# Performance work log

Measured on AMD Instinct MI355X. Metric: run time of the kernel, lower is better.

The kernel has to match this reference:

```python
import jax, jax.numpy as jnp
import numpy as np

N_PIXELS = 262144
N_CENTERS = 1024
N_G = 256

def setup_inputs() -> dict:
    key = jax.random.key(0)
    k1, k2, k3, k4, k5 = jax.random.split(key, 5)
    return {
        "alphas": jax.random.normal(k1, (N_CENTERS, 1), dtype=jnp.float32),
        "betas": jax.random.normal(k2, (N_G, 2), dtype=jnp.float32) * 0.1,
        "K": jax.random.normal(k3, (N_PIXELS, N_G), dtype=jnp.float32) * 0.05,
        "all_pixels": jax.random.normal(k4, (N_PIXELS, 2), dtype=jnp.float32),
        "all_p_centers": jax.random.normal(k5, (N_CENTERS, 2), dtype=jnp.float32),
        "sdp2": jnp.ones((), dtype=jnp.float32) * 2.0,
    }

def reference(alphas, betas, K, all_pixels, all_p_centers, sdp2):
    # deformed pixel coordinates: (n_pixels, 2)
    deformed = all_pixels - K @ betas
    # pairwise squared distances via norm expansion (same math as the torch
    # ones-matmul broadcasting, expressed with plain broadcasting):
    p_norm2 = jnp.sum(jnp.square(deformed), axis=1, keepdims=True)      # (n_pixels, 1)
    c_norm2 = jnp.sum(jnp.square(all_p_centers), axis=1)                # (n_centers,)
    p_dot_c = 2.0 * (deformed @ all_p_centers.T)                        # (n_pixels, n_centers)
    big_matrix = p_norm2 + c_norm2[None, :] - p_dot_c
    kBp = jnp.exp(-big_matrix / (2.0 * sdp2))
    return kBp @ alphas                                                  # (n_pixels, 1)
```

## Files before the change

### kernel.cpp

```cpp
#include <hip/hip_runtime.h>

#if defined(__has_builtin)
#  if __has_builtin(__builtin_amdgcn_exp2f)
#    define EXP2F(x) __builtin_amdgcn_exp2f(x)
#  else
#    define EXP2F(x) exp2f(x)
#  endif
#else
#  define EXP2F(x) exp2f(x)
#endif

constexpr int NPIX  = 262144;
constexpr int NC    = 1024;
constexpr int NG    = 256;
constexpr int BLOCK = 256;
constexpr int PIX_PER_BLOCK = BLOCK * 2;

template <int CTRL>
__device__ __forceinline__ float dpp_add(float v) {
    union { float f; int i; } u, t;
    u.f = v;
    t.i = __builtin_amdgcn_update_dpp(0, u.i, CTRL, 0xF, 0xF, true);
    return v + t.f;
}
__device__ __forceinline__ float sum16(float v) {
    v = dpp_add<0xB1>(v);
    v = dpp_add<0x4E>(v);
    v = dpp_add<0x141>(v);
    v = dpp_add<0x140>(v);
    return v;
}

__global__ __launch_bounds__(BLOCK, 2)
void kbpa_fused(const float* __restrict__ alphas,
                const float* __restrict__ betas,
                const float* __restrict__ K,
                const float* __restrict__ pixels,
                const float* __restrict__ centers,
                const float* __restrict__ sdp2p,
                float* __restrict__ out)
{
    __shared__ float4 cpack[NC];

    const int tid  = threadIdx.x;
    const int lane = tid & 63;
    const int wave = tid >> 6;
    const int l4   = lane & 15;
    const int lg   = lane >> 4;
    const int own  = l4 * 4 + lg;

    const float f   = -1.44269504088896340736f / (2.0f * sdp2p[0]);
    const float m2f = -2.0f * f;

    for (int c = tid; c < NC; c += BLOCK) {
        const float cx = centers[2 * c + 0];
        const float cy = centers[2 * c + 1];
        cpack[c] = make_float4(cx, cy, alphas[c] * EXP2F(f * (cx * cx + cy * cy)), 0.f);
    }

    const float4* bf4 = (const float4*)betas;
    float4 b0[4], b1[4];
    #pragma unroll
    for (int k = 0; k < 4; ++k) {
        b0[k] = bf4[l4 * 2 + k * 32];
        b1[k] = bf4[l4 * 2 + k * 32 + 1];
    }

    const int blockBase = blockIdx.x * PIX_PER_BLOCK;
    const int g0 = blockBase + wave * 64;
    const int g1 = g0 + BLOCK;

    const float2* pix2 = (const float2*)pixels;
    const float2 pixA = pix2[g0 + own];
    const float2 pixB = pix2[g1 + own];

    float dxA = 0.f, dyA = 0.f, dxB = 0.f, dyB = 0.f;
    #pragma unroll 2
    for (int it = 0; it < 16; ++it) {
        const float4* kr = (const float4*)(K + (size_t)(g0 + it * 4 + lg) * NG);
        float4 kv[4];
        #pragma unroll
        for (int k = 0; k < 4; ++k) kv[k] = kr[l4 + 16 * k];
        float sx = 0.f, sy = 0.f;
        #pragma unroll
        for (int k = 0; k < 4; ++k) {
            sx = fmaf(kv[k].x, b0[k].x, sx); sy = fmaf(kv[k].x, b0[k].y, sy);
            sx = fmaf(kv[k].y, b0[k].z, sx); sy = fmaf(kv[k].y, b0[k].w, sy);
            sx = fmaf(kv[k].z, b1[k].x, sx); sy = fmaf(kv[k].z, b1[k].y, sy);
            sx = fmaf(kv[k].w, b1[k].z, sx); sy = fmaf(kv[k].w, b1[k].w, sy);
        }
        sx = sum16(sx); sy = sum16(sy);
        if (l4 == it) { dxA = pixA.x - sx; dyA = pixA.y - sy; }
    }
    #pragma unroll 2
    for (int it = 0; it < 16; ++it) {
        const float4* kr = (const float4*)(K + (size_t)(g1 + it * 4 + lg) * NG);
        float4 kv[4];
        #pragma unroll
        for (int k = 0; k < 4; ++k) kv[k] = kr[l4 + 16 * k];
        float sx = 0.f, sy = 0.f;
        #pragma unroll
        for (int k = 0; k < 4; ++k) {
            sx = fmaf(kv[k].x, b0[k].x, sx); sy = fmaf(kv[k].x, b0[k].y, sy);
            sx = fmaf(kv[k].y, b0[k].z, sx); sy = fmaf(kv[k].y, b0[k].w, sy);
            sx = fmaf(kv[k].z, b1[k].x, sx); sy = fmaf(kv[k].z, b1[k].y, sy);
            sx = fmaf(kv[k].w, b1[k].z, sx); sy = fmaf(kv[k].w, b1[k].w, sy);
        }
        sx = sum16(sx); sy = sum16(sy);
        if (l4 == it) { dxB = pixB.x - sx; dyB = pixB.y - sy; }
    }

    __syncthreads();

    const float dxs0 = m2f * dxA, dys0 = m2f * dyA;
    const float dxs1 = m2f * dxB, dys1 = m2f * dyB;
    const float pn0  = f * (dxA * dxA + dyA * dyA);
    const float pn1  = f * (dxB * dxB + dyB * dyB);
    float acc0 = 0.f, acc1 = 0.f;
    #pragma unroll 8
    for (int c = 0; c < NC; ++c) {
        const float4 cp = cpack[c];
        const float e0 = EXP2F(fmaf(dxs0, cp.x, dys0 * cp.y));
        const float e1 = EXP2F(fmaf(dxs1, cp.x, dys1 * cp.y));
        acc0 = fmaf(cp.z, e0, acc0);
        acc1 = fmaf(cp.z, e1, acc1);
    }
    out[g0 + own] = acc0 * EXP2F(pn0);
    out[g1 + own] = acc1 * EXP2F(pn1);
}

extern "C" void kernel_launch(void* const* d_in, const int* in_sizes, int n_in,
                              void* d_out, int out_size, void* d_ws, size_t ws_size,
                              hipStream_t stream)
{
    const float* alphas  = (const float*)d_in[0];
    const float* betas   = (const float*)d_in[1];
    const float* K       = (const float*)d_in[2];
    const float* pixels  = (const float*)d_in[3];
    const float* centers = (const float*)d_in[4];
    const float* sdp2    = (const float*)d_in[5];
    float* outp          = (float*)d_out;

    hipLaunchKernelGGL(kbpa_fused, dim3(NPIX / PIX_PER_BLOCK), dim3(BLOCK), 0, stream,
                       alphas, betas, K, pixels, centers, sdp2, outp);
}
```

Before: 85.02 us.

## Hold centers in registers and rotate pixels across lanes systolically

```diff
diff --git a/kernel.cpp b/kernel.cpp
--- a/kernel.cpp
+++ b/kernel.cpp
@@ -31,31 +31,70 @@
     return v;
 }
 
+__global__ void prep_centers(const float* __restrict__ alphas,
+                             const float* __restrict__ centers,
+                             const float* __restrict__ sdp2p,
+                             float* __restrict__ ws)
+{
+    const int c = blockIdx.x * blockDim.x + threadIdx.x;
+    if (c < NC) {
+        const float f  = -1.44269504088896340736f / (2.0f * sdp2p[0]);
+        const float cx = centers[2 * c + 0];
+        const float cy = centers[2 * c + 1];
+        ws[c]          = cx;
+        ws[NC + c]     = cy;
+        ws[2 * NC + c] = alphas[c] * EXP2F(f * (cx * cx + cy * cy));
+    }
+}
+
+__device__ __forceinline__ float systolic_b(float dx, float dy, float m2f,
+                                            const float4 rcx[4], const float4 rcy[4],
+                                            const float4 rca[4], int src)
+{
+    float dxs = m2f * dx, dys = m2f * dy, acc = 0.f;
+    for (int t = 0; t < 64; ++t) {
+        #pragma unroll
+        for (int jj = 0; jj < 4; ++jj) {
+            acc = fmaf(rca[jj].x, EXP2F(fmaf(dxs, rcx[jj].x, dys * rcy[jj].x)), acc);
+            acc = fmaf(rca[jj].y, EXP2F(fmaf(dxs, rcx[jj].y, dys * rcy[jj].y)), acc);
+            acc = fmaf(rca[jj].z, EXP2F(fmaf(dxs, rcx[jj].z, dys * rcy[jj].z)), acc);
+            acc = fmaf(rca[jj].w, EXP2F(fmaf(dxs, rcx[jj].w, dys * rcy[jj].w)), acc);
+        }
+        dxs = __shfl(dxs, src);
+        dys = __shfl(dys, src);
+        acc = __shfl(acc, src);
+    }
+    return acc;
+}
+
 __global__ __launch_bounds__(BLOCK, 2)
-void kbpa_fused(const float* __restrict__ alphas,
-                const float* __restrict__ betas,
-                const float* __restrict__ K,
-                const float* __restrict__ pixels,
-                const float* __restrict__ centers,
-                const float* __restrict__ sdp2p,
-                float* __restrict__ out)
+void kbpa_main(const float* __restrict__ betas,
+               const float* __restrict__ K,
+               const float* __restrict__ pixels,
+               const float* __restrict__ sdp2p,
+               const float* __restrict__ ws,
+               float* __restrict__ out)
 {
-    __shared__ float4 cpack[NC];
-
     const int tid  = threadIdx.x;
     const int lane = tid & 63;
     const int wave = tid >> 6;
     const int l4   = lane & 15;
     const int lg   = lane >> 4;
     const int own  = l4 * 4 + lg;
+    const int src  = (lane + 1) & 63;
 
     const float f   = -1.44269504088896340736f / (2.0f * sdp2p[0]);
     const float m2f = -2.0f * f;
 
-    for (int c = tid; c < NC; c += BLOCK) {
-        const float cx = centers[2 * c + 0];
-        const float cy = centers[2 * c + 1];
-        cpack[c] = make_float4(cx, cy, alphas[c] * EXP2F(f * (cx * cx + cy * cy)), 0.f);
+    const float4* wcx4 = (const float4*)(ws);
+    const float4* wcy4 = (const float4*)(ws + NC);
+    const float4* wca4 = (const float4*)(ws + 2 * NC);
+    float4 rcx[4], rcy[4], rca[4];
+    #pragma unroll
+    for (int jj = 0; jj < 4; ++jj) {
+        rcx[jj] = wcx4[lane * 4 + jj];
+        rcy[jj] = wcy4[lane * 4 + jj];
+        rca[jj] = wca4[lane * 4 + jj];
     }
 
     const float4* bf4 = (const float4*)betas;
@@ -74,7 +113,7 @@
     const float2 pixA = pix2[g0 + own];
     const float2 pixB = pix2[g1 + own];
 
-    float dxA = 0.f, dyA = 0.f, dxB = 0.f, dyB = 0.f;
+    float dx0 = 0.f, dy0 = 0.f, dx1 = 0.f, dy1 = 0.f;
     #pragma unroll 2
     for (int it = 0; it < 16; ++it) {
         const float4* kr = (const float4*)(K + (size_t)(g0 + it * 4 + lg) * NG);
@@ -90,8 +129,13 @@
             sx = fmaf(kv[k].w, b1[k].z, sx); sy = fmaf(kv[k].w, b1[k].w, sy);
         }
         sx = sum16(sx); sy = sum16(sy);
-        if (l4 == it) { dxA = pixA.x - sx; dyA = pixA.y - sy; }
+        if (l4 == it) { dx0 = pixA.x - sx; dy0 = pixA.y - sy; }
     }
+
+    const bool early = (wave & 1) == 0;
+    float r0 = 0.f;
+    if (early) r0 = systolic_b(dx0, dy0, m2f, rcx, rcy, rca, src);
+
     #pragma unroll 2
     for (int it = 0; it < 16; ++it) {
         const float4* kr = (const float4*)(K + (size_t)(g1 + it * 4 + lg) * NG);
@@ -107,26 +151,14 @@
             sx = fmaf(kv[k].w, b1[k].z, sx); sy = fmaf(kv[k].w, b1[k].w, sy);
         }
         sx = sum16(sx); sy = sum16(sy);
-        if (l4 == it) { dxB = pixB.x - sx; dyB = pixB.y - sy; }
+        if (l4 == it) { dx1 = pixB.x - sx; dy1 = pixB.y - sy; }
     }
 
-    __syncthreads();
+    if (!early) r0 = systolic_b(dx0, dy0, m2f, rcx, rcy, rca, src);
+    const float r1 = systolic_b(dx1, dy1, m2f, rcx, rcy, rca, src);
 
-    const float dxs0 = m2f * dxA, dys0 = m2f * dyA;
-    const float dxs1 = m2f * dxB, dys1 = m2f * dyB;
-    const float pn0  = f * (dxA * dxA + dyA * dyA);
-    const float pn1  = f * (dxB * dxB + dyB * dyB);
-    float acc0 = 0.f, acc1 = 0.f;
-    #pragma unroll 8
-    for (int c = 0; c < NC; ++c) {
-        const float4 cp = cpack[c];
-        const float e0 = EXP2F(fmaf(dxs0, cp.x, dys0 * cp.y));
-        const float e1 = EXP2F(fmaf(dxs1, cp.x, dys1 * cp.y));
-        acc0 = fmaf(cp.z, e0, acc0);
-        acc1 = fmaf(cp.z, e1, acc1);
-    }
-    out[g0 + own] = acc0 * EXP2F(pn0);
-    out[g1 + own] = acc1 * EXP2F(pn1);
+    out[g0 + own] = r0 * EXP2F(f * (dx0 * dx0 + dy0 * dy0));
+    out[g1 + own] = r1 * EXP2F(f * (dx1 * dx1 + dy1 * dy1));
 }
 
 extern "C" void kernel_launch(void* const* d_in, const int* in_sizes, int n_in,
@@ -140,7 +172,10 @@
     const float* centers = (const float*)d_in[4];
     const float* sdp2    = (const float*)d_in[5];
     float* outp          = (float*)d_out;
+    float* ws            = (float*)d_ws;
 
-    hipLaunchKernelGGL(kbpa_fused, dim3(NPIX / PIX_PER_BLOCK), dim3(BLOCK), 0, stream,
-                       alphas, betas, K, pixels, centers, sdp2, outp);
+    hipLaunchKernelGGL(prep_centers, dim3(NC / 256), dim3(256), 0, stream,
+                       alphas, centers, sdp2, ws);
+    hipLaunchKernelGGL(kbpa_main, dim3(NPIX / PIX_PER_BLOCK), dim3(BLOCK), 0, stream,
+                       betas, K, pixels, sdp2, ws, outp);
 }
```

Result: faster. 80.04 us (-5.9%).

## Split center precompute into separate kernel and read packed centers from global

Applied to the files above, without the earlier changes.

```diff
diff --git a/kernel.cpp b/kernel.cpp
--- a/kernel.cpp
+++ b/kernel.cpp
@@ -14,7 +14,7 @@
 constexpr int NC    = 1024;
 constexpr int NG    = 256;
 constexpr int BLOCK = 256;
-constexpr int PIX_PER_BLOCK = BLOCK * 2;
+constexpr int PIX_PER_BLOCK = 256;
 
 template <int CTRL>
 __device__ __forceinline__ float dpp_add(float v) {
@@ -31,17 +31,28 @@
     return v;
 }
 
-__global__ __launch_bounds__(BLOCK, 2)
-void kbpa_fused(const float* __restrict__ alphas,
-                const float* __restrict__ betas,
-                const float* __restrict__ K,
-                const float* __restrict__ pixels,
-                const float* __restrict__ centers,
-                const float* __restrict__ sdp2p,
-                float* __restrict__ out)
+__global__ void prep_centers(const float* __restrict__ alphas,
+                             const float* __restrict__ centers,
+                             const float* __restrict__ sdp2p,
+                             float4* __restrict__ cpk)
 {
-    __shared__ float4 cpack[NC];
+    const int c = blockIdx.x * blockDim.x + threadIdx.x;
+    if (c < NC) {
+        const float f  = -1.44269504088896340736f / (2.0f * sdp2p[0]);
+        const float cx = centers[2 * c + 0];
+        const float cy = centers[2 * c + 1];
+        cpk[c] = make_float4(cx, cy, alphas[c] * EXP2F(f * (cx * cx + cy * cy)), 0.f);
+    }
+}
 
+__global__ __launch_bounds__(BLOCK, 4)
+void kbpa_main(const float* __restrict__ betas,
+               const float* __restrict__ K,
+               const float* __restrict__ pixels,
+               const float* __restrict__ sdp2p,
+               const float4* __restrict__ cpk,
+               float* __restrict__ out)
+{
     const int tid  = threadIdx.x;
     const int lane = tid & 63;
     const int wave = tid >> 6;
@@ -52,12 +63,6 @@
     const float f   = -1.44269504088896340736f / (2.0f * sdp2p[0]);
     const float m2f = -2.0f * f;
 
-    for (int c = tid; c < NC; c += BLOCK) {
-        const float cx = centers[2 * c + 0];
-        const float cy = centers[2 * c + 1];
-        cpack[c] = make_float4(cx, cy, alphas[c] * EXP2F(f * (cx * cx + cy * cy)), 0.f);
-    }
-
     const float4* bf4 = (const float4*)betas;
     float4 b0[4], b1[4];
     #pragma unroll
@@ -66,15 +71,10 @@
         b1[k] = bf4[l4 * 2 + k * 32 + 1];
     }
 
-    const int blockBase = blockIdx.x * PIX_PER_BLOCK;
-    const int g0 = blockBase + wave * 64;
-    const int g1 = g0 + BLOCK;
+    const int g0 = blockIdx.x * PIX_PER_BLOCK + wave * 64;
+    const float2 mypix = ((const float2*)pixels)[g0 + own];
 
-    const float2* pix2 = (const float2*)pixels;
-    const float2 pixA = pix2[g0 + own];
-    const float2 pixB = pix2[g1 + own];
-
-    float dxA = 0.f, dyA = 0.f, dxB = 0.f, dyB = 0.f;
+    float dx = 0.f, dy = 0.f;
     #pragma unroll 2
     for (int it = 0; it < 16; ++it) {
         const float4* kr = (const float4*)(K + (size_t)(g0 + it * 4 + lg) * NG);
@@ -90,43 +90,31 @@
             sx = fmaf(kv[k].w, b1[k].z, sx); sy = fmaf(kv[k].w, b1[k].w, sy);
         }
         sx = sum16(sx); sy = sum16(sy);
-        if (l4 == it) { dxA = pixA.x - sx; dyA = pixA.y - sy; }
-    }
-    #pragma unroll 2
-    for (int it = 0; it < 16; ++it) {
-        const float4* kr = (const float4*)(K + (size_t)(g1 + it * 4 + lg) * NG);
-        float4 kv[4];
-        #pragma unroll
-        for (int k = 0; k < 4; ++k) kv[k] = kr[l4 + 16 * k];
-        float sx = 0.f, sy = 0.f;
-        #pragma unroll
-        for (int k = 0; k < 4; ++k) {
-            sx = fmaf(kv[k].x, b0[k].x, sx); sy = fmaf(kv[k].x, b0[k].y, sy);
-            sx = fmaf(kv[k].y, b0[k].z, sx); sy = fmaf(kv[k].y, b0[k].w, sy);
-            sx = fmaf(kv[k].z, b1[k].x, sx); sy = fmaf(kv[k].z, b1[k].y, sy);
-            sx = fmaf(kv[k].w, b1[k].z, sx); sy = fmaf(kv[k].w, b1[k].w, sy);
-        }
-        sx = sum16(sx); sy = sum16(sy);
-        if (l4 == it) { dxB = pixB.x - sx; dyB = pixB.y - sy; }
+        if (l4 == it) { dx = mypix.x - sx; dy = mypix.y - sy; }
     }
 
-    __syncthreads();
-
-    const float dxs0 = m2f * dxA, dys0 = m2f * dyA;
-    const float dxs1 = m2f * dxB, dys1 = m2f * dyB;
-    const float pn0  = f * (dxA * dxA + dyA * dyA);
-    const float pn1  = f * (dxB * dxB + dyB * dyB);
-    float acc0 = 0.f, acc1 = 0.f;
-    #pragma unroll 8
-    for (int c = 0; c < NC; ++c) {
-        const float4 cp = cpack[c];
-        const float e0 = EXP2F(fmaf(dxs0, cp.x, dys0 * cp.y));
-        const float e1 = EXP2F(fmaf(dxs1, cp.x, dys1 * cp.y));
-        acc0 = fmaf(cp.z, e0, acc0);
-        acc1 = fmaf(cp.z, e1, acc1);
+    const float dxs = m2f * dx, dys = m2f * dy;
+    const float pn  = f * (dx * dx + dy * dy);
+    float a0 = 0.f, a1 = 0.f, a2 = 0.f, a3 = 0.f;
+    for (int c = 0; c < NC; c += 8) {
+        const float4 q0 = cpk[c + 0];
+        const float4 q1 = cpk[c + 1];
+        const float4 q2 = cpk[c + 2];
+        const float4 q3 = cpk[c + 3];
+        const float4 q4 = cpk[c + 4];
+        const float4 q5 = cpk[c + 5];
+        const float4 q6 = cpk[c + 6];
+        const float4 q7 = cpk[c + 7];
+        a0 = fmaf(q0.z, EXP2F(fmaf(dxs, q0.x, dys * q0.y)), a0);
+        a1 = fmaf(q1.z, EXP2F(fmaf(dxs, q1.x, dys * q1.y)), a1);
+        a2 = fmaf(q2.z, EXP2F(fmaf(dxs, q2.x, dys * q2.y)), a2);
+        a3 = fmaf(q3.z, EXP2F(fmaf(dxs, q3.x, dys * q3.y)), a3);
+        a0 = fmaf(q4.z, EXP2F(fmaf(dxs, q4.x, dys * q4.y)), a0);
+        a1 = fmaf(q5.z, EXP2F(fmaf(dxs, q5.x, dys * q5.y)), a1);
+        a2 = fmaf(q6.z, EXP2F(fmaf(dxs, q6.x, dys * q6.y)), a2);
+        a3 = fmaf(q7.z, EXP2F(fmaf(dxs, q7.x, dys * q7.y)), a3);
     }
-    out[g0 + own] = acc0 * EXP2F(pn0);
-    out[g1 + own] = acc1 * EXP2F(pn1);
+    out[g0 + own] = ((a0 + a1) + (a2 + a3)) * EXP2F(pn);
 }
 
 extern "C" void kernel_launch(void* const* d_in, const int* in_sizes, int n_in,
@@ -140,7 +128,10 @@
     const float* centers = (const float*)d_in[4];
     const float* sdp2    = (const float*)d_in[5];
     float* outp          = (float*)d_out;
+    float4* cpk          = (float4*)d_ws;
 
-    hipLaunchKernelGGL(kbpa_fused, dim3(NPIX / PIX_PER_BLOCK), dim3(BLOCK), 0, stream,
-                       alphas, betas, K, pixels, centers, sdp2, outp);
+    hipLaunchKernelGGL(prep_centers, dim3(NC / 256), dim3(256), 0, stream,
+                       alphas, centers, sdp2, cpk);
+    hipLaunchKernelGGL(kbpa_main, dim3(NPIX / PIX_PER_BLOCK), dim3(BLOCK), 0, stream,
+                       betas, K, pixels, sdp2, cpk, outp);
 }
```

Result: slower. 114.5 us (+34.7%).
